# Kernel tuning notes

Hardware: AMD Instinct MI355X
Metric: run time of the kernel (lower is better)

Reference implementation:

```python
import jax, jax.numpy as jnp
import numpy as np

N_NODES = 100000

def _gcn_conv(x, edge_index, W, b):
    # PyG GCNConv with normalize=False, add_self_loops=False:
    # out[dst] = sum_{(src,dst) in E} (x @ W)[src] + b
    xw = x @ W                                   # [N, out]
    src, dst = edge_index[0], edge_index[1]
    agg = jax.ops.segment_sum(xw[src], dst, num_segments=x.shape[0])  # [N, out]
    return agg + b

def setup_inputs() -> dict:
    key = jax.random.key(0)
    k1, k2, k3, k4 = jax.random.split(key, 4)
    F_in, F_hid, F_out = 128, 64, 40
    E = 1_600_000
    x = jax.random.normal(k1, (N_NODES, F_in), dtype=jnp.float32)
    edge_index = jax.random.randint(k2, (2, E), 0, N_NODES, dtype=jnp.int64)
    W1 = jax.random.normal(k3, (F_in, F_hid), dtype=jnp.float32) * (1.0 / np.sqrt(F_in))
    b1 = jnp.zeros((F_hid,), dtype=jnp.float32)
    W2 = jax.random.normal(k4, (F_hid, F_out), dtype=jnp.float32) * (1.0 / np.sqrt(F_hid))
    b2 = jnp.zeros((F_out,), dtype=jnp.float32)
    return {"x": x, "edge_index": edge_index, "W1": W1, "b1": b1, "W2": W2, "b2": b2}

def reference(x, edge_index, W1, b1, W2, b2):
    h = _gcn_conv(x, edge_index, W1, b1)
    h = jax.nn.relu(h)
    h = _gcn_conv(h, edge_index, W2, b2)
    return jax.nn.log_softmax(h, axis=1)
```

## Files before the change

### kernel.cpp

```cpp
#include <hip/hip_runtime.h>
#include <cstdint>
#include <cstddef>

#define F_IN  128
#define F_HID 64
#define F_OUT 40

#define BSH   9
#define NBMAX 256
#define CHUNK 4096

#define BLD_T   512
#define BLD_CAP 10240

typedef __attribute__((ext_vector_type(8))) short short8;
typedef __attribute__((ext_vector_type(4))) float f32x4;

__device__ __forceinline__ unsigned short f2bf(float f) {
  unsigned u = __float_as_uint(f);
  u += 0x7fffu + ((u >> 16) & 1u);
  return (unsigned short)(u >> 16);
}
__device__ __forceinline__ float bf2f(unsigned short b) {
  return __uint_as_float((unsigned)b << 16);
}
__device__ __forceinline__ float bflo(unsigned u) { return __uint_as_float(u << 16); }
__device__ __forceinline__ float bfhi(unsigned u) { return __uint_as_float(u & 0xffff0000u); }
__device__ __forceinline__ unsigned packbf(float lo, float hi) {
  return (unsigned)f2bf(lo) | ((unsigned)f2bf(hi) << 16);
}

__global__ __launch_bounds__(256) void wcvt_k(const float* __restrict__ W1,
                                              const float* __restrict__ W2,
                                              unsigned short* __restrict__ w1s,
                                              unsigned short* __restrict__ w2s) {
  int t = blockIdx.x * 256 + threadIdx.x;
  int T = gridDim.x * 256;
  for (int i = t; i < 8192; i += T) {
    int f = i >> 9, r = i & 511;
    int lane = r >> 3, j = r & 7;
    int ct = f >> 2, ks = f & 3;
    int n = ct * 16 + (lane & 15);
    int k = ks * 32 + (lane >> 4) * 8 + j;
    w1s[i] = f2bf(W1[k * F_HID + n]);
  }
  for (int i = t; i < 3072; i += T) {
    int f = i >> 9, r = i & 511;
    int lane = r >> 3, j = r & 7;
    int ct = f >> 1, ks = f & 1;
    int n = ct * 16 + (lane & 15);
    int k = ks * 32 + (lane >> 4) * 8 + j;
    w2s[i] = (n < F_OUT) ? f2bf(W2[k * F_OUT + n]) : (unsigned short)0;
  }
}

__global__ __launch_bounds__(256) void front_k(const float* __restrict__ x,
                                               const float* __restrict__ W1,
                                               const unsigned short* __restrict__ w1s,
                                               unsigned short* __restrict__ xw, int N,
                                               const int* __restrict__ ei,
                                               int* __restrict__ counts,
                                               int E, int NBLK, int NBUCK) {
  __shared__ int lh[NBMAX];
  if ((int)blockIdx.x < NBLK) {
    int t = threadIdx.x, blk = blockIdx.x;
    lh[t] = 0;
    __syncthreads();
    int e0 = blk * CHUNK;
    int n = min(CHUNK, E - e0);
    for (int i = t; i < n; i += 256)
      atomicAdd(&lh[((unsigned)ei[E + e0 + i]) >> BSH], 1);
    __syncthreads();
    if (t < NBUCK) counts[t * NBLK + blk] = lh[t];
    return;
  }
  int gblk = blockIdx.x - NBLK;
  int lane = threadIdx.x & 63;
  int wid  = gblk * 4 + (threadIdx.x >> 6);
  int row0 = wid * 16;
  if (row0 >= N) return;
  int m = lane & 15, q = lane >> 4;

  if (row0 + 16 <= N) {
    short8 b[16];
#pragma unroll
    for (int f = 0; f < 16; ++f)
      b[f] = *(const short8*)(w1s + f * 512 + lane * 8);

    short8 a[4];
#pragma unroll
    for (int ks = 0; ks < 4; ++ks) {
      const float* xp = x + (size_t)(row0 + m) * F_IN + ks * 32 + q * 8;
      float4 v0 = *(const float4*)xp;
      float4 v1 = *(const float4*)(xp + 4);
      short8 t;
      t[0] = (short)f2bf(v0.x); t[1] = (short)f2bf(v0.y);
      t[2] = (short)f2bf(v0.z); t[3] = (short)f2bf(v0.w);
      t[4] = (short)f2bf(v1.x); t[5] = (short)f2bf(v1.y);
      t[6] = (short)f2bf(v1.z); t[7] = (short)f2bf(v1.w);
      a[ks] = t;
    }

    f32x4 z = {0.f, 0.f, 0.f, 0.f};
    f32x4 acc[4] = {z, z, z, z};
#pragma unroll
    for (int ct = 0; ct < 4; ++ct)
#pragma unroll
      for (int ks = 0; ks < 4; ++ks)
        acc[ct] = __builtin_amdgcn_mfma_f32_16x16x32_bf16(a[ks], b[ct * 4 + ks],
                                                          acc[ct], 0, 0, 0);
#pragma unroll
    for (int ct = 0; ct < 4; ++ct)
#pragma unroll
      for (int r = 0; r < 4; ++r) {
        int row = row0 + q * 4 + r;
        xw[(size_t)row * F_HID + ct * 16 + m] = f2bf(acc[ct][r]);
      }
  } else {
    for (int r = 0; r < 16 && row0 + r < N; ++r) {
      const float* xr = x + (size_t)(row0 + r) * F_IN;
      float s = 0.f;
      for (int k = 0; k < F_IN; ++k) s = fmaf(xr[k], W1[k * F_HID + lane], s);
      xw[(size_t)(row0 + r) * F_HID + lane] = f2bf(s);
    }
  }
}

__global__ __launch_bounds__(256) void scanA_k(const int* __restrict__ a,
                                               int* __restrict__ psum, int M) {
  int t = threadIdx.x;
  int base = blockIdx.x * 2048 + t * 8;
  int s = 0;
#pragma unroll
  for (int j = 0; j < 8; ++j) if (base + j < M) s += a[base + j];
#pragma unroll
  for (int off = 32; off; off >>= 1) s += __shfl_xor(s, off, 64);
  __shared__ int sm[4];
  if ((t & 63) == 0) sm[t >> 6] = s;
  __syncthreads();
  if (t == 0) psum[blockIdx.x] = sm[0] + sm[1] + sm[2] + sm[3];
}

__global__ __launch_bounds__(256) void scanC_k(int* __restrict__ a,
                                               const int* __restrict__ psum,
                                               int M, int E, int nb) {
  __shared__ int sb[256];
  __shared__ int sm[256];
  int t = threadIdx.x;

  int pv = (t < nb) ? psum[t] : 0;
  sb[t] = pv;
  __syncthreads();
  for (int off = 1; off < 256; off <<= 1) {
    int add = (t >= off) ? sb[t - off] : 0;
    __syncthreads();
    sb[t] += add;
    __syncthreads();
  }
  int excl = sb[t] - pv;
  __syncthreads();
  sb[t] = excl;
  __syncthreads();
  int blockBase = sb[blockIdx.x];

  int base = blockIdx.x * 2048 + t * 8;
  int v[8];
  int s = 0;
#pragma unroll
  for (int j = 0; j < 8; ++j) {
    v[j] = (base + j < M) ? a[base + j] : 0;
    s += v[j];
  }
  sm[t] = s;
  __syncthreads();
  for (int off = 1; off < 256; off <<= 1) {
    int add = (t >= off) ? sm[t - off] : 0;
    __syncthreads();
    sm[t] += add;
    __syncthreads();
  }
  int run = blockBase + sm[t] - s;
#pragma unroll
  for (int j = 0; j < 8; ++j) {
    if (base + j < M) a[base + j] = run;
    run += v[j];
  }
  if (blockIdx.x == 0 && t == 0) a[M] = E;
}

__global__ __launch_bounds__(256) void partition_k(const int* __restrict__ bases,
                                                   const int* __restrict__ ei,
                                                   unsigned* __restrict__ ebuf,
                                                   int E, int NBLK, int NBUCK) {
  __shared__ uint2 slots[CHUNK];
  __shared__ int scn[NBMAX], lcur[NBMAX], gadj[NBMAX];
  int t = threadIdx.x, blk = blockIdx.x;
  int e0 = blk * CHUNK;
  int n = min(CHUNK, E - e0);

  int i0 = t * NBLK + blk;
  int cnt = 0, base0 = 0;
  if (t < NBUCK) {
    base0 = bases[i0];
    cnt = bases[i0 + 1] - base0;
  }
  scn[t] = cnt;
  __syncthreads();
  for (int off = 1; off < 256; off <<= 1) {
    int add = (t >= off) ? scn[t - off] : 0;
    __syncthreads();
    scn[t] += add;
    __syncthreads();
  }
  int excl = scn[t] - cnt;
  if (t < NBUCK) { lcur[t] = excl; gadj[t] = base0 - excl; }
  __syncthreads();

  for (int i = t; i < n; i += 256) {
    int s = ei[e0 + i], d = ei[E + e0 + i];
    int pos = atomicAdd(&lcur[((unsigned)d) >> BSH], 1);
    slots[pos] = make_uint2((unsigned)s, (unsigned)d);
  }
  __syncthreads();
  for (int i = t; i < n; i += 256) {
    uint2 sd = slots[i];
    unsigned pk = ((sd.y & 511u) << 17) | sd.x;
    ebuf[gadj[sd.y >> BSH] + i] = pk;
  }
}

__global__ __launch_bounds__(BLD_T) void build_k(const unsigned* __restrict__ ebuf,
                                                 const int* __restrict__ bases,
                                                 int* __restrict__ row_ptr,
                                                 int* __restrict__ csr,
                                                 int N, int E, int NBLK) {
  __shared__ int hist[512];
  __shared__ int psc[256];
  __shared__ unsigned stg[BLD_CAP];
  int t = threadIdx.x, b = blockIdx.x;
  int nodeBase = b << BSH;
  int S = bases[b * NBLK];
  int T = bases[(b + 1) * NBLK];
  int n = T - S;
  bool useLds = (n <= BLD_CAP);

  if (t < 512) hist[t] = 0;
  __syncthreads();
  for (int i = t; i < n; i += BLD_T) {
    unsigned v = ebuf[S + i];
    if (useLds) stg[i] = v;
    atomicAdd(&hist[v >> 17], 1);
  }
  __syncthreads();

  int v0 = 0, v1 = 0, pair = 0;
  if (t < 256) {
    v0 = hist[2 * t]; v1 = hist[2 * t + 1];
    pair = v0 + v1;
    psc[t] = pair;
  }
  __syncthreads();
  for (int off = 1; off < 256; off <<= 1) {
    int add = (t >= off && t < 256) ? psc[t - off] : 0;
    __syncthreads();
    if (t < 256) psc[t] += add;
    __syncthreads();
  }
  if (t < 256) {
    int ep = psc[t] - pair;
    int e0 = ep, e1 = ep + v0;
    int node0 = nodeBase + 2 * t;
    if (node0 < N) row_ptr[node0] = S + e0;
    if (node0 + 1 < N) row_ptr[node0 + 1] = S + e1;
    hist[2 * t] = e0; hist[2 * t + 1] = e1;
  }
  if (b == 0 && t == 0) row_ptr[N] = E;
  __syncthreads();
  for (int i = t; i < n; i += BLD_T) {
    unsigned v = useLds ? stg[i] : ebuf[S + i];
    int pos = atomicAdd(&hist[v >> 17], 1);
    csr[S + pos] = (int)(v & 0x1FFFFu);
  }
}

__global__ __launch_bounds__(256) void agg1g2_k(const unsigned short* __restrict__ xw,
                                                const int* __restrict__ row_ptr,
                                                const int* __restrict__ csr,
                                                const float* __restrict__ b1,
                                                const unsigned short* __restrict__ w2s,
                                                const float* __restrict__ W2,
                                                unsigned short* __restrict__ hw, int N) {
  __shared__ uint4 hsm[32][8];
  int t = threadIdx.x;
  int wave = t >> 6, lane = t & 63;
  int blockRow0 = blockIdx.x * 32;
  int rowBase = blockRow0 + wave * 8;
  int row = rowBase + (lane >> 3);
  int part = lane & 7;
  bool live = row < N;

  int start = live ? row_ptr[row] : 0;
  int end   = live ? row_ptr[row + 1] : 0;

  float acc[8], bcc[8];
#pragma unroll
  for (int j = 0; j < 8; ++j) { acc[j] = 0.f; bcc[j] = 0.f; }

  int i = start;
  for (; i + 1 < end; i += 2) {
    int s0 = csr[i];
    int s1 = csr[i + 1];
    uint4 v0 = *(const uint4*)(xw + ((size_t)s0 << 6) + (part << 3));
    uint4 v1 = *(const uint4*)(xw + ((size_t)s1 << 6) + (part << 3));
    acc[0] += bflo(v0.x); acc[1] += bfhi(v0.x);
    acc[2] += bflo(v0.y); acc[3] += bfhi(v0.y);
    acc[4] += bflo(v0.z); acc[5] += bfhi(v0.z);
    acc[6] += bflo(v0.w); acc[7] += bfhi(v0.w);
    bcc[0] += bflo(v1.x); bcc[1] += bfhi(v1.x);
    bcc[2] += bflo(v1.y); bcc[3] += bfhi(v1.y);
    bcc[4] += bflo(v1.z); bcc[5] += bfhi(v1.z);
    bcc[6] += bflo(v1.w); bcc[7] += bfhi(v1.w);
  }
  if (i < end) {
    int s = csr[i];
    uint4 v = *(const uint4*)(xw + ((size_t)s << 6) + (part << 3));
    acc[0] += bflo(v.x); acc[1] += bfhi(v.x);
    acc[2] += bflo(v.y); acc[3] += bfhi(v.y);
    acc[4] += bflo(v.z); acc[5] += bfhi(v.z);
    acc[6] += bflo(v.w); acc[7] += bfhi(v.w);
  }

  if (live) {
    int c0 = part << 3;
    float4 bA = *(const float4*)(b1 + c0);
    float4 bB = *(const float4*)(b1 + c0 + 4);
    float r0 = fmaxf(acc[0] + bcc[0] + bA.x, 0.f);
    float r1 = fmaxf(acc[1] + bcc[1] + bA.y, 0.f);
    float r2 = fmaxf(acc[2] + bcc[2] + bA.z, 0.f);
    float r3 = fmaxf(acc[3] + bcc[3] + bA.w, 0.f);
    float r4 = fmaxf(acc[4] + bcc[4] + bB.x, 0.f);
    float r5 = fmaxf(acc[5] + bcc[5] + bB.y, 0.f);
    float r6 = fmaxf(acc[6] + bcc[6] + bB.z, 0.f);
    float r7 = fmaxf(acc[7] + bcc[7] + bB.w, 0.f);
    uint4 o = make_uint4(packbf(r0, r1), packbf(r2, r3), packbf(r4, r5), packbf(r6, r7));
    int lr = row - blockRow0;
    hsm[lr][part ^ (lr & 7)] = o;
  }
  __syncthreads();

  if (wave < 2) {
    int frow0 = blockRow0 + wave * 16;
    if (frow0 >= N) return;
    int m = lane & 15, q = lane >> 4;
    if (frow0 + 16 <= N) {
      short8 b[6];
#pragma unroll
      for (int f = 0; f < 6; ++f)
        b[f] = *(const short8*)(w2s + f * 512 + lane * 8);
      short8 a[2];
#pragma unroll
      for (int ks = 0; ks < 2; ++ks) {
        int lr = wave * 16 + m;
        int p = ks * 4 + q;
        a[ks] = *(const short8*)&hsm[lr][p ^ (lr & 7)];
      }
      f32x4 z = {0.f, 0.f, 0.f, 0.f};
      f32x4 acc2[3] = {z, z, z};
#pragma unroll
      for (int ct = 0; ct < 3; ++ct)
#pragma unroll
        for (int ks = 0; ks < 2; ++ks)
          acc2[ct] = __builtin_amdgcn_mfma_f32_16x16x32_bf16(a[ks], b[ct * 2 + ks],
                                                             acc2[ct], 0, 0, 0);
#pragma unroll
      for (int ct = 0; ct < 3; ++ct)
#pragma unroll
        for (int r = 0; r < 4; ++r) {
          int row2 = frow0 + q * 4 + r;
          int c = ct * 16 + m;
          if (c < F_OUT) hw[(size_t)row2 * F_OUT + c] = f2bf(acc2[ct][r]);
        }
    } else {
      for (int r = 0; r < 16; ++r) {
        int row2 = frow0 + r;
        if (row2 >= N) break;
        if (lane < F_OUT) {
          int lr = wave * 16 + r;
          float s = 0.f;
          for (int k = 0; k < F_HID; ++k) {
            const unsigned short* hp =
                (const unsigned short*)&hsm[lr][(k >> 3) ^ (lr & 7)];
            s = fmaf(bf2f(hp[k & 7]), W2[k * F_OUT + lane], s);
          }
          hw[(size_t)row2 * F_OUT + lane] = f2bf(s);
        }
      }
    }
  }
}

__global__ __launch_bounds__(256) void agg2_ls_k(const unsigned short* __restrict__ hw,
                                                 const int* __restrict__ row_ptr,
                                                 const int* __restrict__ csr,
                                                 const float* __restrict__ b2,
                                                 float* __restrict__ out, int N) {
  int wid = (blockIdx.x * 256 + threadIdx.x) >> 6;
  int lane = threadIdx.x & 63;
  int rowBase = wid * 8;
  if (rowBase >= N) return;
  int row = rowBase + (lane >> 3);
  int part = lane & 7;
  bool live = row < N;
  bool ld = live && (part < 5);

  int start = live ? row_ptr[row] : 0;
  int end   = live ? row_ptr[row + 1] : 0;

  float acc[8], bcc[8];
#pragma unroll
  for (int j = 0; j < 8; ++j) { acc[j] = 0.f; bcc[j] = 0.f; }

  int i = start;
  for (; i + 1 < end; i += 2) {
    int s0 = csr[i];
    int s1 = csr[i + 1];
    if (ld) {
      uint4 v0 = *(const uint4*)(hw + (size_t)s0 * F_OUT + (part << 3));
      uint4 v1 = *(const uint4*)(hw + (size_t)s1 * F_OUT + (part << 3));
      acc[0] += bflo(v0.x); acc[1] += bfhi(v0.x);
      acc[2] += bflo(v0.y); acc[3] += bfhi(v0.y);
      acc[4] += bflo(v0.z); acc[5] += bfhi(v0.z);
      acc[6] += bflo(v0.w); acc[7] += bfhi(v0.w);
      bcc[0] += bflo(v1.x); bcc[1] += bfhi(v1.x);
      bcc[2] += bflo(v1.y); bcc[3] += bfhi(v1.y);
      bcc[4] += bflo(v1.z); bcc[5] += bfhi(v1.z);
      bcc[6] += bflo(v1.w); bcc[7] += bfhi(v1.w);
    }
  }
  if (i < end && ld) {
    int s = csr[i];
    uint4 v = *(const uint4*)(hw + (size_t)s * F_OUT + (part << 3));
    acc[0] += bflo(v.x); acc[1] += bfhi(v.x);
    acc[2] += bflo(v.y); acc[3] += bfhi(v.y);
    acc[4] += bflo(v.z); acc[5] += bfhi(v.z);
    acc[6] += bflo(v.w); acc[7] += bfhi(v.w);
  }

  bool valid = ld;
  float vj[8];
  float m = -3.4e38f;
  if (valid) {
    int c0 = part << 3;
    float4 bA = *(const float4*)(b2 + c0);
    float4 bB = *(const float4*)(b2 + c0 + 4);
    vj[0] = acc[0] + bcc[0] + bA.x; vj[1] = acc[1] + bcc[1] + bA.y;
    vj[2] = acc[2] + bcc[2] + bA.z; vj[3] = acc[3] + bcc[3] + bA.w;
    vj[4] = acc[4] + bcc[4] + bB.x; vj[5] = acc[5] + bcc[5] + bB.y;
    vj[6] = acc[6] + bcc[6] + bB.z; vj[7] = acc[7] + bcc[7] + bB.w;
#pragma unroll
    for (int j = 0; j < 8; ++j) m = fmaxf(m, vj[j]);
  }
#pragma unroll
  for (int off = 1; off < 8; off <<= 1) m = fmaxf(m, __shfl_xor(m, off, 64));
  float ex = 0.f;
  if (valid) {
#pragma unroll
    for (int j = 0; j < 8; ++j) ex += __expf(vj[j] - m);
  }
#pragma unroll
  for (int off = 1; off < 8; off <<= 1) ex += __shfl_xor(ex, off, 64);
  float lse = __logf(ex) + m;

  if (valid) {
    int c0 = part << 3;
    float* op = out + (size_t)row * F_OUT + c0;
    *(float4*)op = make_float4(vj[0] - lse, vj[1] - lse, vj[2] - lse, vj[3] - lse);
    *(float4*)(op + 4) = make_float4(vj[4] - lse, vj[5] - lse, vj[6] - lse, vj[7] - lse);
  }
}

extern "C" void kernel_launch(void* const* d_in, const int* in_sizes, int n_in,
                              void* d_out, int out_size, void* d_ws, size_t ws_size,
                              hipStream_t stream) {
  const float* x  = (const float*)d_in[0];
  const int*   ei = (const int*)d_in[1];
  const float* W1 = (const float*)d_in[2];
  const float* b1 = (const float*)d_in[3];
  const float* W2 = (const float*)d_in[4];
  const float* b2 = (const float*)d_in[5];

  int N = in_sizes[0] / F_IN;
  int E = in_sizes[1] / 2;

  char* base = (char*)d_ws;
  size_t szA = (size_t)N * F_HID * sizeof(unsigned short);
  size_t szEb = (size_t)E * sizeof(unsigned);
  size_t szHw = (size_t)N * F_OUT * sizeof(unsigned short);
  size_t szB = (szEb > szHw) ? szEb : szHw;
  unsigned short* xw = (unsigned short*)base;
  char* regB = base + ((szA + 255) & ~(size_t)255);
  unsigned* ebuf       = (unsigned*)regB;
  unsigned short* hw   = (unsigned short*)regB;
  int* row_ptr = (int*)(regB + ((szB + 255) & ~(size_t)255));
  int* csr     = row_ptr + N + 1;
  int* counts  = csr + E;
  float* out = (float*)d_out;

  int aggGrid  = (N * 8 + 255) / 256;
  int gemmGrid = (N + 63) / 64;
  int fusGrid  = (N + 31) / 32;
  int NBLK  = (E + CHUNK - 1) / CHUNK;
  int NBUCK = (N + 511) >> BSH;
  int M = NBUCK * NBLK;
  int* psum = counts + M + 1;
  unsigned short* w1s = (unsigned short*)(psum + 256);
  unsigned short* w2s = w1s + 8192;
  int scanBlocks = (M + 2047) / 2048;

  wcvt_k<<<44, 256, 0, stream>>>(W1, W2, w1s, w2s);

  front_k<<<NBLK + gemmGrid, 256, 0, stream>>>(x, W1, w1s, xw, N,
                                               ei, counts, E, NBLK, NBUCK);

  scanA_k<<<scanBlocks, 256, 0, stream>>>(counts, psum, M);
  scanC_k<<<scanBlocks, 256, 0, stream>>>(counts, psum, M, E, scanBlocks);
  partition_k<<<NBLK, 256, 0, stream>>>(counts, ei, ebuf, E, NBLK, NBUCK);
  build_k<<<NBUCK, BLD_T, 0, stream>>>(ebuf, counts, row_ptr, csr, N, E, NBLK);

  agg1g2_k<<<fusGrid, 256, 0, stream>>>(xw, row_ptr, csr, b1, w2s, W2, hw, N);
  agg2_ls_k<<<aggGrid, 256, 0, stream>>>(hw, row_ptr, csr, b2, out, N);
}
```

Baseline: 218.4 us.

## Fold weight conversion into front kernel and unroll CSR gathers by four

Removes the separate weight-conversion launch. Each GEMM block now converts W1 to the bf16 MFMA layout in shared memory itself, and histogram block 0 converts W2 into the global buffer consumed later. This saves one kernel launch and its dependency, at the cost of every GEMM block redundantly reading and converting W1 and using 16KB of LDS, which may reduce occupancy. The two aggregation kernels also unroll the neighbor gather loop from two to four loads to raise memory-level parallelism.

```diff
diff --git a/kernel.cpp b/kernel.cpp
--- a/kernel.cpp
+++ b/kernel.cpp
@@ -30,40 +30,20 @@
   return (unsigned)f2bf(lo) | ((unsigned)f2bf(hi) << 16);
 }
 
-__global__ __launch_bounds__(256) void wcvt_k(const float* __restrict__ W1,
-                                              const float* __restrict__ W2,
-                                              unsigned short* __restrict__ w1s,
-                                              unsigned short* __restrict__ w2s) {
-  int t = blockIdx.x * 256 + threadIdx.x;
-  int T = gridDim.x * 256;
-  for (int i = t; i < 8192; i += T) {
-    int f = i >> 9, r = i & 511;
-    int lane = r >> 3, j = r & 7;
-    int ct = f >> 2, ks = f & 3;
-    int n = ct * 16 + (lane & 15);
-    int k = ks * 32 + (lane >> 4) * 8 + j;
-    w1s[i] = f2bf(W1[k * F_HID + n]);
-  }
-  for (int i = t; i < 3072; i += T) {
-    int f = i >> 9, r = i & 511;
-    int lane = r >> 3, j = r & 7;
-    int ct = f >> 1, ks = f & 1;
-    int n = ct * 16 + (lane & 15);
-    int k = ks * 32 + (lane >> 4) * 8 + j;
-    w2s[i] = (n < F_OUT) ? f2bf(W2[k * F_OUT + n]) : (unsigned short)0;
-  }
-}
-
 __global__ __launch_bounds__(256) void front_k(const float* __restrict__ x,
                                                const float* __restrict__ W1,
-                                               const unsigned short* __restrict__ w1s,
+                                               const float* __restrict__ W2,
+                                               unsigned short* __restrict__ w2s,
                                                unsigned short* __restrict__ xw, int N,
                                                const int* __restrict__ ei,
                                                int* __restrict__ counts,
                                                int E, int NBLK, int NBUCK) {
   __shared__ int lh[NBMAX];
+  __shared__ unsigned short w1l[8192];
+  int t = threadIdx.x;
+
   if ((int)blockIdx.x < NBLK) {
-    int t = threadIdx.x, blk = blockIdx.x;
+    int blk = blockIdx.x;
     lh[t] = 0;
     __syncthreads();
     int e0 = blk * CHUNK;
@@ -72,11 +52,39 @@
       atomicAdd(&lh[((unsigned)ei[E + e0 + i]) >> BSH], 1);
     __syncthreads();
     if (t < NBUCK) counts[t * NBLK + blk] = lh[t];
+    if (blk == 0) {
+      for (int i = t; i < 3072; i += 256) {
+        int f = i >> 9, r = i & 511;
+        int lane = r >> 3, j = r & 7;
+        int ct = f >> 1, ks = f & 1;
+        int n2 = ct * 16 + (lane & 15);
+        int k = ks * 32 + (lane >> 4) * 8 + j;
+        w2s[i] = (n2 < F_OUT) ? f2bf(W2[k * F_OUT + n2]) : (unsigned short)0;
+      }
+    }
     return;
   }
+
+  {
+    int k = t >> 1, n0 = (t & 1) * 32;
+    const float4* wp = (const float4*)(W1 + k * F_HID + n0);
+    float4 v[8];
+#pragma unroll
+    for (int u = 0; u < 8; ++u) v[u] = wp[u];
+#pragma unroll
+    for (int u = 0; u < 32; ++u) {
+      int n = n0 + u;
+      float f = ((const float*)v)[u];
+      int idx = ((n >> 4) * 4 + (k >> 5)) * 512 +
+                (((k >> 3) & 3) * 16 + (n & 15)) * 8 + (k & 7);
+      w1l[idx] = f2bf(f);
+    }
+  }
+  __syncthreads();
+
   int gblk = blockIdx.x - NBLK;
-  int lane = threadIdx.x & 63;
-  int wid  = gblk * 4 + (threadIdx.x >> 6);
+  int lane = t & 63;
+  int wid  = gblk * 4 + (t >> 6);
   int row0 = wid * 16;
   if (row0 >= N) return;
   int m = lane & 15, q = lane >> 4;
@@ -85,7 +93,7 @@
     short8 b[16];
 #pragma unroll
     for (int f = 0; f < 16; ++f)
-      b[f] = *(const short8*)(w1s + f * 512 + lane * 8);
+      b[f] = *(const short8*)(w1l + f * 512 + lane * 8);
 
     short8 a[4];
 #pragma unroll
@@ -93,12 +101,12 @@
       const float* xp = x + (size_t)(row0 + m) * F_IN + ks * 32 + q * 8;
       float4 v0 = *(const float4*)xp;
       float4 v1 = *(const float4*)(xp + 4);
-      short8 t;
-      t[0] = (short)f2bf(v0.x); t[1] = (short)f2bf(v0.y);
-      t[2] = (short)f2bf(v0.z); t[3] = (short)f2bf(v0.w);
-      t[4] = (short)f2bf(v1.x); t[5] = (short)f2bf(v1.y);
-      t[6] = (short)f2bf(v1.z); t[7] = (short)f2bf(v1.w);
-      a[ks] = t;
+      short8 tt;
+      tt[0] = (short)f2bf(v0.x); tt[1] = (short)f2bf(v0.y);
+      tt[2] = (short)f2bf(v0.z); tt[3] = (short)f2bf(v0.w);
+      tt[4] = (short)f2bf(v1.x); tt[5] = (short)f2bf(v1.y);
+      tt[6] = (short)f2bf(v1.z); tt[7] = (short)f2bf(v1.w);
+      a[ks] = tt;
     }
 
     f32x4 z = {0.f, 0.f, 0.f, 0.f};
@@ -307,11 +315,15 @@
   for (int j = 0; j < 8; ++j) { acc[j] = 0.f; bcc[j] = 0.f; }
 
   int i = start;
-  for (; i + 1 < end; i += 2) {
+  for (; i + 3 < end; i += 4) {
     int s0 = csr[i];
     int s1 = csr[i + 1];
+    int s2 = csr[i + 2];
+    int s3 = csr[i + 3];
     uint4 v0 = *(const uint4*)(xw + ((size_t)s0 << 6) + (part << 3));
     uint4 v1 = *(const uint4*)(xw + ((size_t)s1 << 6) + (part << 3));
+    uint4 v2 = *(const uint4*)(xw + ((size_t)s2 << 6) + (part << 3));
+    uint4 v3 = *(const uint4*)(xw + ((size_t)s3 << 6) + (part << 3));
     acc[0] += bflo(v0.x); acc[1] += bfhi(v0.x);
     acc[2] += bflo(v0.y); acc[3] += bfhi(v0.y);
     acc[4] += bflo(v0.z); acc[5] += bfhi(v0.z);
@@ -320,8 +332,16 @@
     bcc[2] += bflo(v1.y); bcc[3] += bfhi(v1.y);
     bcc[4] += bflo(v1.z); bcc[5] += bfhi(v1.z);
     bcc[6] += bflo(v1.w); bcc[7] += bfhi(v1.w);
-  }
-  if (i < end) {
+    acc[0] += bflo(v2.x); acc[1] += bfhi(v2.x);
+    acc[2] += bflo(v2.y); acc[3] += bfhi(v2.y);
+    acc[4] += bflo(v2.z); acc[5] += bfhi(v2.z);
+    acc[6] += bflo(v2.w); acc[7] += bfhi(v2.w);
+    bcc[0] += bflo(v3.x); bcc[1] += bfhi(v3.x);
+    bcc[2] += bflo(v3.y); bcc[3] += bfhi(v3.y);
+    bcc[4] += bflo(v3.z); bcc[5] += bfhi(v3.z);
+    bcc[6] += bflo(v3.w); bcc[7] += bfhi(v3.w);
+  }
+  for (; i < end; ++i) {
     int s = csr[i];
     uint4 v = *(const uint4*)(xw + ((size_t)s << 6) + (part << 3));
     acc[0] += bflo(v.x); acc[1] += bfhi(v.x);
@@ -421,12 +441,16 @@
   for (int j = 0; j < 8; ++j) { acc[j] = 0.f; bcc[j] = 0.f; }
 
   int i = start;
-  for (; i + 1 < end; i += 2) {
+  for (; i + 3 < end; i += 4) {
     int s0 = csr[i];
     int s1 = csr[i + 1];
+    int s2 = csr[i + 2];
+    int s3 = csr[i + 3];
     if (ld) {
       uint4 v0 = *(const uint4*)(hw + (size_t)s0 * F_OUT + (part << 3));
       uint4 v1 = *(const uint4*)(hw + (size_t)s1 * F_OUT + (part << 3));
+      uint4 v2 = *(const uint4*)(hw + (size_t)s2 * F_OUT + (part << 3));
+      uint4 v3 = *(const uint4*)(hw + (size_t)s3 * F_OUT + (part << 3));
       acc[0] += bflo(v0.x); acc[1] += bfhi(v0.x);
       acc[2] += bflo(v0.y); acc[3] += bfhi(v0.y);
       acc[4] += bflo(v0.z); acc[5] += bfhi(v0.z);
@@ -435,15 +459,25 @@
       bcc[2] += bflo(v1.y); bcc[3] += bfhi(v1.y);
       bcc[4] += bflo(v1.z); bcc[5] += bfhi(v1.z);
       bcc[6] += bflo(v1.w); bcc[7] += bfhi(v1.w);
-    }
-  }
-  if (i < end && ld) {
+      acc[0] += bflo(v2.x); acc[1] += bfhi(v2.x);
+      acc[2] += bflo(v2.y); acc[3] += bfhi(v2.y);
+      acc[4] += bflo(v2.z); acc[5] += bfhi(v2.z);
+      acc[6] += bflo(v2.w); acc[7] += bfhi(v2.w);
+      bcc[0] += bflo(v3.x); bcc[1] += bfhi(v3.x);
+      bcc[2] += bflo(v3.y); bcc[3] += bfhi(v3.y);
+      bcc[4] += bflo(v3.z); bcc[5] += bfhi(v3.z);
+      bcc[6] += bflo(v3.w); bcc[7] += bfhi(v3.w);
+    }
+  }
+  for (; i < end; ++i) {
     int s = csr[i];
-    uint4 v = *(const uint4*)(hw + (size_t)s * F_OUT + (part << 3));
-    acc[0] += bflo(v.x); acc[1] += bfhi(v.x);
-    acc[2] += bflo(v.y); acc[3] += bfhi(v.y);
-    acc[4] += bflo(v.z); acc[5] += bfhi(v.z);
-    acc[6] += bflo(v.w); acc[7] += bfhi(v.w);
+    if (ld) {
+      uint4 v = *(const uint4*)(hw + (size_t)s * F_OUT + (part << 3));
+      acc[0] += bflo(v.x); acc[1] += bfhi(v.x);
+      acc[2] += bflo(v.y); acc[3] += bfhi(v.y);
+      acc[4] += bflo(v.z); acc[5] += bfhi(v.z);
+      acc[6] += bflo(v.w); acc[7] += bfhi(v.w);
+    }
   }
 
   bool valid = ld;
@@ -513,13 +547,10 @@
   int NBUCK = (N + 511) >> BSH;
   int M = NBUCK * NBLK;
   int* psum = counts + M + 1;
-  unsigned short* w1s = (unsigned short*)(psum + 256);
-  unsigned short* w2s = w1s + 8192;
+  unsigned short* w2s = (unsigned short*)(psum + 256);
   int scanBlocks = (M + 2047) / 2048;
 
-  wcvt_k<<<44, 256, 0, stream>>>(W1, W2, w1s, w2s);
-
-  front_k<<<NBLK + gemmGrid, 256, 0, stream>>>(x, W1, w1s, xw, N,
+  front_k<<<NBLK + gemmGrid, 256, 0, stream>>>(x, W1, W2, w2s, xw, N,
                                                ei, counts, E, NBLK, NBUCK);
 
   scanA_k<<<scanBlocks, 256, 0, stream>>>(counts, psum, M);
```

New measurement: 218.4 us. No clear change (-0.0%).
